# Kernel optimization log

Measured on AMD Instinct MI355X. Metric: run time of the kernel, lower is better.

## Reference

```python
import jax, jax.numpy as jnp
import numpy as np

K = 5
BASE_LAMBDA = 0.05
BASE_DELTA = 0.01
TV_ITERS = 3
TV_STEP = 0.2
LAMBDA_RANGE = (0.5, 1.5)
JITTER = 0.1
FUSION_SCALE = 2.0
BETA_T = 0.02
BETA_S = 0.01
BETA_MIN = 0.0
BETA_MAX = 1.0
EPS = 1e-8


def _gen_param_sets():
    # Deterministic replication of SGSv2Config._generate_param_sets
    rng = np.random.RandomState(0)
    ps = [(0.0, 0.0, 0, 0.0)]
    lmin = BASE_LAMBDA * LAMBDA_RANGE[0]
    lmax = BASE_LAMBDA * LAMBDA_RANGE[1]
    for i in range(K - 1):
        lb = lmin + (lmax - lmin) * i / max(1, K - 2)
        jit = rng.uniform(-JITTER, JITTER)
        li = max(0.0, lb * (1 + jit))
        di = BASE_DELTA * float(np.sqrt(li / (BASE_LAMBDA + 1e-8)))
        ps.append((float(li), di, TV_ITERS, TV_STEP))
    return ps

PARAM_SETS = _gen_param_sets()


def lower_median(v, axis):
    # torch.median semantics: lower of the two middle values for even n
    s = jnp.sort(v, axis=axis)
    n = v.shape[axis]
    return jnp.take(s, (n - 1) // 2, axis=axis)


def huber_tv(x, lam, delta, iters, step):
    # Anisotropic Huber-TV, skip_clamp=True (artifact path)
    xd = x
    for _ in range(iters):
        dx = jnp.pad(xd[:, :, :, 1:] - xd[:, :, :, :-1], ((0, 0), (0, 0), (0, 0), (0, 1)))
        dy = jnp.pad(xd[:, :, 1:, :] - xd[:, :, :-1, :], ((0, 0), (0, 0), (0, 1), (0, 0)))
        gx = dx / (delta + jnp.abs(dx))
        gy = dy / (delta + jnp.abs(dy))
        div_x = gx - jnp.pad(gx[:, :, :, :-1], ((0, 0), (0, 0), (0, 0), (1, 0)))
        div_y = gy - jnp.pad(gy[:, :, :-1, :], ((0, 0), (0, 0), (1, 0), (0, 0)))
        xd = xd - step * (xd - x - lam * (div_x + div_y))
    return xd


def setup_inputs() -> dict:
    key = jax.random.key(0)
    x = jax.random.normal(key, (32, 3, 256, 256), dtype=jnp.float32)
    return {"x": x}


def reference(x):
    B = x.shape[0]
    # per-sample artifact scale: median of |x| over (C,H,W)
    scale = lower_median(jnp.abs(x).reshape(B, -1), axis=1).reshape(B, 1, 1, 1) + EPS
    x_norm = x / scale
    views = [x]
    for k in range(1, K):
        lam, delta, iters, step = PARAM_SETS[k]
        views.append(huber_tv(x_norm, lam, delta, iters, step) * scale)
    stack = jnp.stack(views, axis=0)  # [K,B,C,H,W]
    med = lower_median(stack, axis=0)  # K odd -> true median
    dev = jnp.abs(stack - med[None])
    mad = lower_median(dev, axis=0)
    mad = jnp.maximum(mad, 0.1 * mad.mean())
    w = jnp.exp(-dev / (FUSION_SCALE * mad[None]))
    fused = (w * stack).sum(axis=0) / (w.sum(axis=0) + EPS)
    # adaptive beta (corruption detection)
    D = dev.mean(axis=(0, 2, 3, 4)).reshape(-1, 1, 1, 1)
    beta = BETA_MIN + (BETA_MAX - BETA_MIN) * jax.nn.sigmoid((D - BETA_T) / BETA_S)
    return fused, beta
```

## Files before the change

### kernel.cpp

```cpp
#include <hip/hip_runtime.h>
#include <hip/hip_fp16.h>
#include <math.h>

#define B_ 32
#define C_ 3
#define H_ 256
#define W_ 256
#define HW_ 65536
#define CHW_ 196608
#define TOT_ 6291456

#define VIEWS_OFF_B 0ull
#define GHIST_OFF_B (4ull * TOT_ * 2ull)
#define STATE_OFF_B (GHIST_OFF_B + 32ull*2048*4)
#define SCALE_OFF_B (STATE_OFF_B + 32ull*8)
#define PMAD_OFF_B  (SCALE_OFF_B + 32ull*4)
#define PDEV_OFF_B  (PMAD_OFF_B + 384ull*4)
#define MEAN_OFF_B  (PDEV_OFF_B + 384ull*4)

#define RC_ 32
#define RB5_ 5
#define NW_ 8
#define NBAND_ 8

__device__ __forceinline__ float g_of(float d, float delta) {
    return d * __builtin_amdgcn_rcpf(delta + fabsf(d));
}
__device__ __forceinline__ void cswap(float& a, float& b) {
    float lo = fminf(a, b), hi = fmaxf(a, b); a = lo; b = hi;
}
__device__ __forceinline__ float median5(float a0, float a1, float a2, float a3, float a4) {
    cswap(a0,a1); cswap(a3,a4); cswap(a2,a4); cswap(a2,a3); cswap(a0,a3);
    cswap(a0,a2); cswap(a1,a4); cswap(a1,a3); cswap(a1,a2);
    return a2;
}

__device__ __forceinline__ float4 loadv4(const __half* p) {
    union { float2 f; __half2 h[2]; } u;
    u.f = *(const float2*)p;
    float2 lo = __half22float2(u.h[0]), hi = __half22float2(u.h[1]);
    return make_float4(lo.x, lo.y, hi.x, hi.y);
}

__global__ void k_init(unsigned* state) {
    int t = threadIdx.x;
    if (t < 32) { state[2*t] = 0u; state[2*t+1] = 98303u; }
}

__global__ __launch_bounds__(256) void k_hist(const float* __restrict__ x,
                                              unsigned* __restrict__ ghist,
                                              const unsigned* __restrict__ state,
                                              unsigned matchmask, int shift) {
    __shared__ unsigned h[2048];
    int t = threadIdx.x, chunk = blockIdx.x, s = blockIdx.y;
    #pragma unroll
    for (int i = 0; i < 8; i++) h[t + 256*i] = 0u;
    __syncthreads();
    unsigned prefix = state[2*s];
    size_t base = (size_t)s*CHW_ + (size_t)chunk*4096;
    #pragma unroll
    for (int i = 0; i < 16; i++) {
        float v = x[base + i*256 + t];
        unsigned u = __float_as_uint(fabsf(v));
        if ((u & matchmask) == prefix) atomicAdd(&h[(u >> shift) & 2047u], 1u);
    }
    __syncthreads();
    #pragma unroll
    for (int i = 0; i < 8; i++) {
        unsigned c = h[t + 256*i];
        if (c) atomicAdd(&ghist[s*2048 + t + 256*i], c);
    }
}

__global__ __launch_bounds__(256) void k_select(unsigned* __restrict__ ghist,
                                                unsigned* __restrict__ state,
                                                float* __restrict__ scale,
                                                int shift, int final_pass) {
    __shared__ unsigned sc[256];
    int t = threadIdx.x, s = blockIdx.x;
    unsigned krem = state[2*s+1];
    unsigned v[8]; unsigned ts = 0;
    #pragma unroll
    for (int i = 0; i < 8; i++) { v[i] = ghist[s*2048 + t*8 + i]; ts += v[i]; }
    sc[t] = ts; __syncthreads();
    for (int off = 1; off < 256; off <<= 1) {
        unsigned a = sc[t];
        unsigned b = (t >= off) ? sc[t-off] : 0u;
        __syncthreads();
        sc[t] = a + b;
        __syncthreads();
    }
    unsigned incl = sc[t], base = incl - ts;
    if (ts > 0 && base <= krem && krem < incl) {
        unsigned c = base; int dig = -1; unsigned nk = 0;
        #pragma unroll
        for (int i = 0; i < 8; i++) {
            if (dig < 0) {
                if (krem < c + v[i]) { dig = t*8 + i; nk = krem - c; }
                else c += v[i];
            }
        }
        unsigned prefix = state[2*s] | ((unsigned)dig << shift);
        state[2*s] = prefix;
        state[2*s+1] = nk;
        if (final_pass) scale[s] = __uint_as_float(prefix) + 1e-8f;
    }
    #pragma unroll
    for (int i = 0; i < 8; i++) ghist[s*2048 + t*8 + i] = 0u;
}

#define LDXN(r) loadv4(&xnl[wr0 + (r)][col])

#define STEP(r, nxt) { \
    float4 a = s##r; float4 vn = nxt; \
    float vn3 = __shfl(a.x, lnext); \
    float g0 = g_of(a.y - a.x, del); \
    float g1 = g_of(a.z - a.y, del); \
    float g2 = g_of(a.w - a.z, del); \
    float g3 = g_of(vn3 - a.w, del); g3 = is63 ? 0.f : g3; \
    float gxl = __shfl(g3, lprev); gxl = is0 ? 0.f : gxl; \
    float4 gy; gy.x = g_of(vn.x - a.x, del); gy.y = g_of(vn.y - a.y, del); \
    gy.z = g_of(vn.z - a.z, del); gy.w = g_of(vn.w - a.w, del); \
    float4 xr = LDXN(r); \
    a.x = fmaf(-0.2f, fmaf(-lam, (g0 - gxl) + (gy.x - gprev.x), a.x - xr.x), a.x); \
    a.y = fmaf(-0.2f, fmaf(-lam, (g1 - g0)  + (gy.y - gprev.y), a.y - xr.y), a.y); \
    a.z = fmaf(-0.2f, fmaf(-lam, (g2 - g1)  + (gy.z - gprev.z), a.z - xr.z), a.z); \
    a.w = fmaf(-0.2f, fmaf(-lam, (g3 - g2)  + (gy.w - gprev.w), a.w - xr.w), a.w); \
    s##r = a; gprev = gy; }

#define STOREROW5(r) { int wr = wr0 + r; \
    if (wr >= 4 && wr < 4 + RC_) { int gi = i0 + wr - 4; \
        union { __half2 h[2]; float2 f; } pk; \
        pk.h[0] = __floats2half2_rn(s##r.x * sc, s##r.y * sc); \
        pk.h[1] = __floats2half2_rn(s##r.z * sc, s##r.w * sc); \
        *(float2*)(vout + (size_t)gi*W_ + col) = pk.f; } }

__global__ __launch_bounds__(512) void k_views(const float* __restrict__ x,
        __half* __restrict__ views, const float* __restrict__ scale,
        float l0, float l1, float l2, float l3,
        float e0, float e1, float e2, float e3) {
    __shared__ __align__(16) __half xnl[40][256];
    __shared__ float exch[NW_][2][256];
    const int t = threadIdx.x, lane = t & 63, wv = t >> 6;
    const int band = blockIdx.x, bc = blockIdx.y, b = bc / 3;
    const int i0 = band * RC_;
    const float sc = scale[b], inv_sc = 1.0f / sc;
    const float* img = x + (size_t)bc * HW_;
    const int wr0 = wv * RB5_, col = lane << 2;
    const bool topblk = (band == 0), botblk = (band == NBAND_ - 1);
    const bool is0 = (lane == 0), is63 = (lane == 63);
    const int lnext = is63 ? 63 : lane + 1;
    const int lprev = is0 ? 0 : lane - 1;

    #pragma unroll
    for (int r = 0; r < RB5_; r++) {
        int gi = i0 - 4 + wr0 + r; gi = gi < 0 ? 0 : (gi > 255 ? 255 : gi);
        float4 v = *(const float4*)(img + gi * W_ + col);
        union { __half2 h[2]; float2 f; } pk;
        pk.h[0] = __floats2half2_rn(v.x * inv_sc, v.y * inv_sc);
        pk.h[1] = __floats2half2_rn(v.z * inv_sc, v.w * inv_sc);
        *(float2*)&xnl[wr0 + r][col] = pk.f;
    }
    __syncthreads();

    float4 s0, s1, s2, s3, s4, gt, gb;

    #pragma unroll 1
    for (int view = 0; view < 4; view++) {
        const float lam = (view == 0) ? l0 : (view == 1) ? l1 : (view == 2) ? l2 : l3;
        const float del = (view == 0) ? e0 : (view == 1) ? e1 : (view == 2) ? e2 : e3;
        s0 = LDXN(0); s1 = LDXN(1); s2 = LDXN(2); s3 = LDXN(3); s4 = LDXN(4);
        gt = (wv == 0)       ? s0 : LDXN(-1);
        gb = (wv == NW_ - 1) ? s4 : LDXN(5);

        #pragma unroll 1
        for (int it = 0; it < 3; it++) {
            float4 gprev;
            gprev.x = g_of(s0.x - gt.x, del);
            gprev.y = g_of(s0.y - gt.y, del);
            gprev.z = g_of(s0.z - gt.z, del);
            gprev.w = g_of(s0.w - gt.w, del);
            STEP(0, s1) STEP(1, s2) STEP(2, s3) STEP(3, s4) STEP(4, gb)
            if (it < 2) {
                __syncthreads();
                *(float4*)&exch[wv][0][col] = s0;
                *(float4*)&exch[wv][1][col] = s4;
                __syncthreads();
                gt = wv ? *(const float4*)&exch[wv - 1][1][col] : s0;
                gb = (wv < NW_ - 1) ? *(const float4*)&exch[wv + 1][0][col] : s4;
                if (topblk && wv == 0)       { s0 = s4; s1 = s4; s2 = s4; s3 = s4; gt = s4; }
                if (botblk && wv == NW_ - 1) { s1 = s0; s2 = s0; s3 = s0; s4 = s0; gb = s0; }
            }
        }
        __half* vout = views + (size_t)view * TOT_ + (size_t)bc * HW_;
        STOREROW5(0) STOREROW5(1) STOREROW5(2) STOREROW5(3) STOREROW5(4)
    }
}

__global__ __launch_bounds__(256) void k_stats(const float* __restrict__ x,
                                               const __half* __restrict__ views,
                                               float* __restrict__ pmad,
                                               float* __restrict__ pdev) {
    int t = threadIdx.x, chunk = blockIdx.x, b = blockIdx.y;
    float am = 0.f, ad = 0.f;
    for (int i = 0; i < 16; i++) {
        size_t px = (size_t)b*CHW_ + ((size_t)chunk*4096 + i*256 + t) * 4;
        float4 a0 = *(const float4*)(x + px);
        float4 a1 = loadv4(views + px);
        float4 a2 = loadv4(views + TOT_ + px);
        float4 a3 = loadv4(views + 2ull*TOT_ + px);
        float4 a4 = loadv4(views + 3ull*TOT_ + px);
        const float* q0 = &a0.x; const float* q1 = &a1.x; const float* q2 = &a2.x;
        const float* q3 = &a3.x; const float* q4 = &a4.x;
        #pragma unroll
        for (int j = 0; j < 4; j++) {
            float s0 = q0[j], s1 = q1[j], s2 = q2[j], s3 = q3[j], s4 = q4[j];
            float med = median5(s0, s1, s2, s3, s4);
            float d0 = fabsf(s0-med), d1 = fabsf(s1-med), d2 = fabsf(s2-med),
                  d3 = fabsf(s3-med), d4 = fabsf(s4-med);
            am += median5(d0, d1, d2, d3, d4);
            ad += d0 + d1 + d2 + d3 + d4;
        }
    }
    __shared__ float r[256];
    r[t] = am; __syncthreads();
    for (int off = 128; off > 0; off >>= 1) { if (t < off) r[t] += r[t+off]; __syncthreads(); }
    if (t == 0) pmad[b*12 + chunk] = r[0];
    __syncthreads();
    r[t] = ad; __syncthreads();
    for (int off = 128; off > 0; off >>= 1) { if (t < off) r[t] += r[t+off]; __syncthreads(); }
    if (t == 0) pdev[b*12 + chunk] = r[0];
}

__global__ __launch_bounds__(256) void k_final(const float* __restrict__ pmad,
                                               const float* __restrict__ pdev,
                                               float* __restrict__ meanp,
                                               float* __restrict__ out_beta) {
    __shared__ float r[256];
    int t = threadIdx.x;
    float s = 0.f;
    for (int j = t; j < 384; j += 256) s += pmad[j];
    r[t] = s; __syncthreads();
    for (int off = 128; off > 0; off >>= 1) { if (t < off) r[t] += r[t+off]; __syncthreads(); }
    if (t == 0) meanp[0] = r[0] / (float)TOT_;
    if (t < 32) {
        float sd = 0.f;
        for (int j = 0; j < 12; j++) sd += pdev[t*12 + j];
        float D = sd / (5.0f * (float)CHW_);
        float z = (D - 0.02f) / 0.01f;
        out_beta[t] = 1.0f / (1.0f + __expf(-z));
    }
}

__global__ __launch_bounds__(256) void k_fuse(const float* __restrict__ x,
                                              const __half* __restrict__ views,
                                              const float* __restrict__ meanp,
                                              float* __restrict__ out) {
    int t = threadIdx.x;
    float floorv = 0.1f * meanp[0];
    for (int i = 0; i < 16; i++) {
        size_t px = ((size_t)blockIdx.x*4096 + i*256 + t) * 4;
        float4 a0 = *(const float4*)(x + px);
        float4 a1 = loadv4(views + px);
        float4 a2 = loadv4(views + TOT_ + px);
        float4 a3 = loadv4(views + 2ull*TOT_ + px);
        float4 a4 = loadv4(views + 3ull*TOT_ + px);
        const float* q0 = &a0.x; const float* q1 = &a1.x; const float* q2 = &a2.x;
        const float* q3 = &a3.x; const float* q4 = &a4.x;
        float4 o;
        float* qo = &o.x;
        #pragma unroll
        for (int j = 0; j < 4; j++) {
            float s0 = q0[j], s1 = q1[j], s2 = q2[j], s3 = q3[j], s4 = q4[j];
            float med = median5(s0, s1, s2, s3, s4);
            float d0 = fabsf(s0-med), d1 = fabsf(s1-med), d2 = fabsf(s2-med),
                  d3 = fabsf(s3-med), d4 = fabsf(s4-med);
            float mad = median5(d0, d1, d2, d3, d4);
            float madf = fmaxf(mad, floorv);
            float inv = 1.0f / (2.0f * madf);
            float w0 = __expf(-d0*inv), w1 = __expf(-d1*inv), w2 = __expf(-d2*inv),
                  w3 = __expf(-d3*inv), w4 = __expf(-d4*inv);
            float num = w0*s0 + w1*s1 + w2*s2 + w3*s3 + w4*s4;
            float den = w0 + w1 + w2 + w3 + w4 + 1e-8f;
            qo[j] = num / den;
        }
        *(float4*)(out + px) = o;
    }
}

extern "C" void kernel_launch(void* const* d_in, const int* in_sizes, int n_in,
                              void* d_out, int out_size, void* d_ws, size_t ws_size,
                              hipStream_t stream) {
    const float* x = (const float*)d_in[0];
    float* out = (float*)d_out;
    char* ws = (char*)d_ws;
    __half*   views = (__half*)(ws + VIEWS_OFF_B);
    unsigned* ghist = (unsigned*)(ws + GHIST_OFF_B);
    unsigned* state = (unsigned*)(ws + STATE_OFF_B);
    float*    scale = (float*)(ws + SCALE_OFF_B);
    float*    pmad  = (float*)(ws + PMAD_OFF_B);
    float*    pdev  = (float*)(ws + PDEV_OFF_B);
    float*    meanp = (float*)(ws + MEAN_OFF_B);

    const double s4h[4] = {0.5488135039273248, 0.7151893663724195,
                           0.6027633760716439, 0.5448831829968969};
    float lam[4], del[4];
    for (int i = 0; i < 4; i++) {
        double lb  = 0.025 + (0.075 - 0.025) * (double)i / 3.0;
        double jit = -0.1 + 0.2 * s4h[i];
        double li  = lb * (1.0 + jit);
        if (li < 0.0) li = 0.0;
        double di  = 0.01 * sqrt(li / (0.05 + 1e-8));
        lam[i] = (float)li; del[i] = (float)di;
    }

    hipMemsetAsync(ghist, 0, 32*2048*4, stream);
    k_init<<<1, 64, 0, stream>>>(state);

    k_hist  <<<dim3(48,32), 256, 0, stream>>>(x, ghist, state, 0u,          21);
    k_select<<<32,          256, 0, stream>>>(ghist, state, scale, 21, 0);
    k_hist  <<<dim3(48,32), 256, 0, stream>>>(x, ghist, state, 0xFFE00000u, 10);
    k_select<<<32,          256, 0, stream>>>(ghist, state, scale, 10, 0);
    k_hist  <<<dim3(48,32), 256, 0, stream>>>(x, ghist, state, 0xFFFFFC00u, 0);
    k_select<<<32,          256, 0, stream>>>(ghist, state, scale, 0, 1);

    k_views<<<dim3(NBAND_,96), 512, 0, stream>>>(x, views, scale,
                                                 lam[0], lam[1], lam[2], lam[3],
                                                 del[0], del[1], del[2], del[3]);
    k_stats<<<dim3(12,32), 256, 0, stream>>>(x, views, pmad, pdev);
    k_final<<<1,           256, 0, stream>>>(pmad, pdev, meanp, out + TOT_);
    k_fuse <<<384,         256, 0, stream>>>(x, views, meanp, out);
    (void)in_sizes; (void)n_in; (void)out_size; (void)ws_size;
}
```

Before: 147.3 us.

## Compact median candidates after first radix pass; split TV views across grid z

The per-sample median radix select now makes one full histogram pass over x. It then compacts the elements that match the 11-bit prefix into a candidate buffer, and a single finish kernel resolves the remaining two digit passes from that small list. This replaces two full re-reads of x plus their launches. Separately, the TV denoise kernel launches one block per view (grid z = 4) instead of looping over views inside a block, which raises parallelism but reloads and renormalizes the input band four times. The risk is that the finish kernel runs serially in 32 blocks if many elements share the prefix.

```diff
diff --git a/kernel.cpp b/kernel.cpp
--- a/kernel.cpp
+++ b/kernel.cpp
@@ -11,8 +11,11 @@
 #define TOT_ 6291456
 
 #define VIEWS_OFF_B 0ull
-#define GHIST_OFF_B (4ull * TOT_ * 2ull)
-#define STATE_OFF_B (GHIST_OFF_B + 32ull*2048*4)
+#define CAND_OFF_B  (4ull * TOT_ * 2ull)
+#define CAND_SZ_B   (32ull * 48 * 4096 * 4)
+#define GHIST_OFF_B (CAND_OFF_B + CAND_SZ_B)
+#define CNT_OFF_B   (GHIST_OFF_B + 32ull*2048*4)
+#define STATE_OFF_B (CNT_OFF_B + 32ull*48*4)
 #define SCALE_OFF_B (STATE_OFF_B + 32ull*8)
 #define PMAD_OFF_B  (SCALE_OFF_B + 32ull*4)
 #define PDEV_OFF_B  (PMAD_OFF_B + 384ull*4)
@@ -107,6 +110,112 @@
     }
     #pragma unroll
     for (int i = 0; i < 8; i++) ghist[s*2048 + t*8 + i] = 0u;
+}
+
+__global__ __launch_bounds__(256) void k_compact(const float* __restrict__ x,
+                                                 const unsigned* __restrict__ state,
+                                                 unsigned* __restrict__ cnt,
+                                                 unsigned* __restrict__ cand) {
+    __shared__ unsigned lcnt;
+    int t = threadIdx.x, chunk = blockIdx.x, s = blockIdx.y;
+    if (t == 0) lcnt = 0u;
+    __syncthreads();
+    unsigned prefix = state[2*s];
+    size_t base = (size_t)s*CHW_ + (size_t)chunk*4096;
+    unsigned* dst = cand + ((size_t)s*48 + chunk)*4096;
+    #pragma unroll
+    for (int i = 0; i < 16; i++) {
+        float v = x[base + i*256 + t];
+        unsigned u = __float_as_uint(fabsf(v));
+        if ((u & 0xFFE00000u) == prefix) {
+            unsigned o = atomicAdd(&lcnt, 1u);
+            dst[o] = u;
+        }
+    }
+    __syncthreads();
+    if (t == 0) cnt[s*48 + chunk] = lcnt;
+}
+
+__global__ __launch_bounds__(256) void k_finish(const unsigned* __restrict__ cnt,
+                                                const unsigned* __restrict__ state,
+                                                const unsigned* __restrict__ cand,
+                                                float* __restrict__ scale) {
+    __shared__ unsigned hist[2048];
+    __shared__ unsigned sc[256];
+    __shared__ unsigned bdig, bk;
+    int t = threadIdx.x, s = blockIdx.x;
+    unsigned prefix = state[2*s], krem = state[2*s+1];
+    for (int i = t; i < 2048; i += 256) hist[i] = 0u;
+    __syncthreads();
+    for (int c = 0; c < 48; c++) {
+        int n = (int)cnt[s*48 + c];
+        const unsigned* lst = cand + ((size_t)s*48 + c)*4096;
+        for (int i = t; i < n; i += 256) atomicAdd(&hist[(lst[i] >> 10) & 2047u], 1u);
+    }
+    __syncthreads();
+    {
+        unsigned v[8]; unsigned ts = 0;
+        #pragma unroll
+        for (int i = 0; i < 8; i++) { v[i] = hist[t*8 + i]; ts += v[i]; }
+        sc[t] = ts; __syncthreads();
+        for (int off = 1; off < 256; off <<= 1) {
+            unsigned a = sc[t];
+            unsigned b = (t >= off) ? sc[t-off] : 0u;
+            __syncthreads();
+            sc[t] = a + b;
+            __syncthreads();
+        }
+        unsigned incl = sc[t], base = incl - ts;
+        if (ts > 0 && base <= krem && krem < incl) {
+            unsigned c = base; int dig = -1; unsigned nk = 0;
+            #pragma unroll
+            for (int i = 0; i < 8; i++) {
+                if (dig < 0) {
+                    if (krem < c + v[i]) { dig = t*8 + i; nk = krem - c; }
+                    else c += v[i];
+                }
+            }
+            bdig = (unsigned)dig; bk = nk;
+        }
+    }
+    __syncthreads();
+    unsigned p22 = prefix | (bdig << 10), krem2 = bk;
+    for (int i = t; i < 1024; i += 256) hist[i] = 0u;
+    __syncthreads();
+    for (int c = 0; c < 48; c++) {
+        int n = (int)cnt[s*48 + c];
+        const unsigned* lst = cand + ((size_t)s*48 + c)*4096;
+        for (int i = t; i < n; i += 256) {
+            unsigned u = lst[i];
+            if ((u & 0xFFFFFC00u) == p22) atomicAdd(&hist[u & 1023u], 1u);
+        }
+    }
+    __syncthreads();
+    {
+        unsigned v[4]; unsigned ts = 0;
+        #pragma unroll
+        for (int i = 0; i < 4; i++) { v[i] = hist[t*4 + i]; ts += v[i]; }
+        sc[t] = ts; __syncthreads();
+        for (int off = 1; off < 256; off <<= 1) {
+            unsigned a = sc[t];
+            unsigned b = (t >= off) ? sc[t-off] : 0u;
+            __syncthreads();
+            sc[t] = a + b;
+            __syncthreads();
+        }
+        unsigned incl = sc[t], base = incl - ts;
+        if (ts > 0 && base <= krem2 && krem2 < incl) {
+            unsigned c = base; int dig = -1;
+            #pragma unroll
+            for (int i = 0; i < 4; i++) {
+                if (dig < 0) {
+                    if (krem2 < c + v[i]) dig = t*4 + i;
+                    else c += v[i];
+                }
+            }
+            scale[s] = __uint_as_float(p22 | (unsigned)dig) + 1e-8f;
+        }
+    }
 }
 
 #define LDXN(r) loadv4(&xnl[wr0 + (r)][col])
@@ -143,6 +252,9 @@
     __shared__ float exch[NW_][2][256];
     const int t = threadIdx.x, lane = t & 63, wv = t >> 6;
     const int band = blockIdx.x, bc = blockIdx.y, b = bc / 3;
+    const int view = blockIdx.z;
+    const float lam = (view == 0) ? l0 : (view == 1) ? l1 : (view == 2) ? l2 : l3;
+    const float del = (view == 0) ? e0 : (view == 1) ? e1 : (view == 2) ? e2 : e3;
     const int i0 = band * RC_;
     const float sc = scale[b], inv_sc = 1.0f / sc;
     const float* img = x + (size_t)bc * HW_;
@@ -164,37 +276,31 @@
     __syncthreads();
 
     float4 s0, s1, s2, s3, s4, gt, gb;
+    s0 = LDXN(0); s1 = LDXN(1); s2 = LDXN(2); s3 = LDXN(3); s4 = LDXN(4);
+    gt = (wv == 0)       ? s0 : LDXN(-1);
+    gb = (wv == NW_ - 1) ? s4 : LDXN(5);
 
     #pragma unroll 1
-    for (int view = 0; view < 4; view++) {
-        const float lam = (view == 0) ? l0 : (view == 1) ? l1 : (view == 2) ? l2 : l3;
-        const float del = (view == 0) ? e0 : (view == 1) ? e1 : (view == 2) ? e2 : e3;
-        s0 = LDXN(0); s1 = LDXN(1); s2 = LDXN(2); s3 = LDXN(3); s4 = LDXN(4);
-        gt = (wv == 0)       ? s0 : LDXN(-1);
-        gb = (wv == NW_ - 1) ? s4 : LDXN(5);
-
-        #pragma unroll 1
-        for (int it = 0; it < 3; it++) {
-            float4 gprev;
-            gprev.x = g_of(s0.x - gt.x, del);
-            gprev.y = g_of(s0.y - gt.y, del);
-            gprev.z = g_of(s0.z - gt.z, del);
-            gprev.w = g_of(s0.w - gt.w, del);
-            STEP(0, s1) STEP(1, s2) STEP(2, s3) STEP(3, s4) STEP(4, gb)
-            if (it < 2) {
-                __syncthreads();
-                *(float4*)&exch[wv][0][col] = s0;
-                *(float4*)&exch[wv][1][col] = s4;
-                __syncthreads();
-                gt = wv ? *(const float4*)&exch[wv - 1][1][col] : s0;
-                gb = (wv < NW_ - 1) ? *(const float4*)&exch[wv + 1][0][col] : s4;
-                if (topblk && wv == 0)       { s0 = s4; s1 = s4; s2 = s4; s3 = s4; gt = s4; }
-                if (botblk && wv == NW_ - 1) { s1 = s0; s2 = s0; s3 = s0; s4 = s0; gb = s0; }
-            }
-        }
-        __half* vout = views + (size_t)view * TOT_ + (size_t)bc * HW_;
-        STOREROW5(0) STOREROW5(1) STOREROW5(2) STOREROW5(3) STOREROW5(4)
-    }
+    for (int it = 0; it < 3; it++) {
+        float4 gprev;
+        gprev.x = g_of(s0.x - gt.x, del);
+        gprev.y = g_of(s0.y - gt.y, del);
+        gprev.z = g_of(s0.z - gt.z, del);
+        gprev.w = g_of(s0.w - gt.w, del);
+        STEP(0, s1) STEP(1, s2) STEP(2, s3) STEP(3, s4) STEP(4, gb)
+        if (it < 2) {
+            __syncthreads();
+            *(float4*)&exch[wv][0][col] = s0;
+            *(float4*)&exch[wv][1][col] = s4;
+            __syncthreads();
+            gt = wv ? *(const float4*)&exch[wv - 1][1][col] : s0;
+            gb = (wv < NW_ - 1) ? *(const float4*)&exch[wv + 1][0][col] : s4;
+            if (topblk && wv == 0)       { s0 = s4; s1 = s4; s2 = s4; s3 = s4; gt = s4; }
+            if (botblk && wv == NW_ - 1) { s1 = s0; s2 = s0; s3 = s0; s4 = s0; gb = s0; }
+        }
+    }
+    __half* vout = views + (size_t)view * TOT_ + (size_t)bc * HW_;
+    STOREROW5(0) STOREROW5(1) STOREROW5(2) STOREROW5(3) STOREROW5(4)
 }
 
 __global__ __launch_bounds__(256) void k_stats(const float* __restrict__ x,
@@ -295,7 +401,9 @@
     float* out = (float*)d_out;
     char* ws = (char*)d_ws;
     __half*   views = (__half*)(ws + VIEWS_OFF_B);
+    unsigned* cand  = (unsigned*)(ws + CAND_OFF_B);
     unsigned* ghist = (unsigned*)(ws + GHIST_OFF_B);
+    unsigned* cnt   = (unsigned*)(ws + CNT_OFF_B);
     unsigned* state = (unsigned*)(ws + STATE_OFF_B);
     float*    scale = (float*)(ws + SCALE_OFF_B);
     float*    pmad  = (float*)(ws + PMAD_OFF_B);
@@ -317,16 +425,14 @@
     hipMemsetAsync(ghist, 0, 32*2048*4, stream);
     k_init<<<1, 64, 0, stream>>>(state);
 
-    k_hist  <<<dim3(48,32), 256, 0, stream>>>(x, ghist, state, 0u,          21);
-    k_select<<<32,          256, 0, stream>>>(ghist, state, scale, 21, 0);
-    k_hist  <<<dim3(48,32), 256, 0, stream>>>(x, ghist, state, 0xFFE00000u, 10);
-    k_select<<<32,          256, 0, stream>>>(ghist, state, scale, 10, 0);
-    k_hist  <<<dim3(48,32), 256, 0, stream>>>(x, ghist, state, 0xFFFFFC00u, 0);
-    k_select<<<32,          256, 0, stream>>>(ghist, state, scale, 0, 1);
-
-    k_views<<<dim3(NBAND_,96), 512, 0, stream>>>(x, views, scale,
-                                                 lam[0], lam[1], lam[2], lam[3],
-                                                 del[0], del[1], del[2], del[3]);
+    k_hist   <<<dim3(48,32), 256, 0, stream>>>(x, ghist, state, 0u, 21);
+    k_select <<<32,          256, 0, stream>>>(ghist, state, scale, 21, 0);
+    k_compact<<<dim3(48,32), 256, 0, stream>>>(x, state, cnt, cand);
+    k_finish <<<32,          256, 0, stream>>>(cnt, state, cand, scale);
+
+    k_views<<<dim3(NBAND_,96,4), 512, 0, stream>>>(x, views, scale,
+                                                   lam[0], lam[1], lam[2], lam[3],
+                                                   del[0], del[1], del[2], del[3]);
     k_stats<<<dim3(12,32), 256, 0, stream>>>(x, views, pmad, pdev);
     k_final<<<1,           256, 0, stream>>>(pmad, pdev, meanp, out + TOT_);
     k_fuse <<<384,         256, 0, stream>>>(x, views, meanp, out);
```

After: 181.5 us. +23.3%, slower.
